# Kernel optimization log

Hardware: AMD Instinct MI355X
Metric: run time of the kernel (lower is better)

The kernel has to match this reference:

```python
import jax, jax.numpy as jnp
import numpy as np

HSS = 1024            # hidden_state_size
SEQ = 8               # mamba_seq_size (forced: HSS//SEQ*8 must equal HSS)
HID = HSS // SEQ * 8  # mamba d_model = 1024
REWARD = 2
BATCH = 256
D_INNER = 2 * HID     # mamba expand=2
HEADDIM = 64
NHEADS = D_INNER // HEADDIM
DSTATE = 128
DCONV = 4
CONV_DIM = D_INNER + 2 * DSTATE


def _mamba_layer_params(key, scale):
    k = jax.random.split(key, 5)
    d_in_proj = 2 * D_INNER + 2 * DSTATE + NHEADS
    return (
        jax.random.normal(k[0], (HID, d_in_proj)) * scale,                       # in_proj
        jax.random.normal(k[1], (CONV_DIM, DCONV)) * scale,                      # depthwise conv weight
        jnp.zeros((CONV_DIM,)),                                                  # conv bias
        jax.random.normal(k[2], (NHEADS,)) * 0.5,                                # dt_bias
        jnp.log(jax.random.uniform(k[3], (NHEADS,), minval=1.0, maxval=16.0)),   # A_log
        jnp.ones((NHEADS,)),                                                     # D skip
        jnp.ones((D_INNER,)),                                                    # gated-RMSNorm weight
        jax.random.normal(k[4], (D_INNER, HID)) * scale,                         # out_proj
    )


def setup_inputs() -> dict:
    key = jax.random.key(0)
    ks = jax.random.split(key, 8)
    s = 0.02
    inp = {"x": jax.random.normal(ks[0], (BATCH, HSS), dtype=jnp.float32)}
    inp["w_in1"] = jax.random.normal(ks[1], (HSS, HSS * SEQ)) * s
    inp["b_in1"] = jnp.zeros((HSS * SEQ,))
    inp["w_in2"] = jax.random.normal(ks[2], (HSS * SEQ, HSS * SEQ)) * s
    inp["b_in2"] = jnp.zeros((HSS * SEQ,))
    for i, k in ((1, ks[3]), (2, ks[4])):
        (inp[f"m{i}_in_proj"], inp[f"m{i}_conv_w"], inp[f"m{i}_conv_b"],
         inp[f"m{i}_dt_bias"], inp[f"m{i}_A_log"], inp[f"m{i}_D"],
         inp[f"m{i}_norm_w"], inp[f"m{i}_out_proj"]) = _mamba_layer_params(k, s)
    inp["w_out1"] = jax.random.normal(ks[5], (HID * SEQ, HID)) * s
    inp["b_out1"] = jnp.zeros((HID,))
    inp["w_out2"] = jax.random.normal(ks[6], (HID, REWARD)) * s
    inp["b_out2"] = jnp.zeros((REWARD,))
    return inp


def _mamba2(x, in_proj, conv_w, conv_b, dt_bias, A_log, Dp, norm_w, out_proj):
    # x: (B, L, HID). Mamba2 block (ngroups=1) with sequential selective scan.
    Bb, L, _ = x.shape
    zxbcdt = x @ in_proj
    z = zxbcdt[..., :D_INNER]
    xBC = zxbcdt[..., D_INNER:D_INNER + CONV_DIM]
    dt = zxbcdt[..., D_INNER + CONV_DIM:]                       # (B, L, H)
    # causal depthwise conv, kernel DCONV
    xp = jnp.pad(xBC, ((0, 0), (DCONV - 1, 0), (0, 0)))
    xBC = sum(xp[:, k:k + L, :] * conv_w[:, k] for k in range(DCONV)) + conv_b
    xBC = jax.nn.silu(xBC)
    xs = xBC[..., :D_INNER].reshape(Bb, L, NHEADS, HEADDIM)
    Bm = xBC[..., D_INNER:D_INNER + DSTATE]                     # (B, L, S)
    Cm = xBC[..., D_INNER + DSTATE:]                            # (B, L, S)
    dt = jax.nn.softplus(dt + dt_bias)
    dA = jnp.exp(dt * (-jnp.exp(A_log)))                        # (B, L, H)

    def step(h, ins):
        dA_t, dt_t, x_t, B_t, C_t = ins
        # h: (B, H, P, S)
        h = dA_t[:, :, None, None] * h + (dt_t[:, :, None] * x_t)[..., None] * B_t[:, None, None, :]
        y = jnp.einsum('bhps,bs->bhp', h, C_t)
        return h, y

    h0 = jnp.zeros((Bb, NHEADS, HEADDIM, DSTATE), x.dtype)
    ins = (dA.transpose(1, 0, 2), dt.transpose(1, 0, 2), xs.transpose(1, 0, 2, 3),
           Bm.transpose(1, 0, 2), Cm.transpose(1, 0, 2))
    _, ys = jax.lax.scan(step, h0, ins)                          # ys: (L, B, H, P)
    y = ys.transpose(1, 0, 2, 3) + xs * Dp[:, None]
    # gated RMSNorm: rmsnorm(y * silu(z)) * weight
    y = y.reshape(Bb, L, D_INNER) * jax.nn.silu(z)
    y = y * jax.lax.rsqrt(jnp.mean(y * y, axis=-1, keepdims=True) + 1e-5) * norm_w
    return y @ out_proj


def reference(x, w_in1, b_in1, w_in2, b_in2,
              m1_in_proj, m1_conv_w, m1_conv_b, m1_dt_bias, m1_A_log, m1_D, m1_norm_w, m1_out_proj,
              m2_in_proj, m2_conv_w, m2_conv_b, m2_dt_bias, m2_A_log, m2_D, m2_norm_w, m2_out_proj,
              w_out1, b_out1, w_out2, b_out2):
    b = x.shape[0]
    h = jax.nn.relu(x @ w_in1 + b_in1) @ w_in2 + b_in2          # mlp_in
    h = h.reshape(b, SEQ, HID)
    h = _mamba2(h, m1_in_proj, m1_conv_w, m1_conv_b, m1_dt_bias, m1_A_log, m1_D, m1_norm_w, m1_out_proj)
    h = _mamba2(h, m2_in_proj, m2_conv_w, m2_conv_b, m2_dt_bias, m2_A_log, m2_D, m2_norm_w, m2_out_proj)
    h = h.reshape(b, SEQ * HID)
    return jax.nn.relu(h @ w_out1 + b_out1) @ w_out2 + b_out2   # mlp_out
```

## Files before the change

kernel.cpp:

```cpp
#include <hip/hip_runtime.h>

#define BATCHN 256
#define SEQL   8
#define HIDN   1024
#define DIN    2048
#define NH     32
#define HDIM   64
#define DST    128
#define CONVD  2304
#define DPROJ  4384
#define DPROJP 4480
#define ROWS   2048

typedef float f32x4 __attribute__((ext_vector_type(4)));
typedef short bf16x8 __attribute__((ext_vector_type(8)));

__device__ __forceinline__ ushort f2bf(float f) {
    unsigned x = __float_as_uint(f);
    unsigned r = (x + 0x7fffu + ((x >> 16) & 1u)) >> 16;
    return (ushort)r;
}
__device__ __forceinline__ float bf2f(ushort u) {
    return __uint_as_float(((unsigned)u) << 16);
}

#define GL2LDS(g, l)                                                        \
    __builtin_amdgcn_global_load_lds(                                       \
        (const __attribute__((address_space(1))) void*)(g),                 \
        (__attribute__((address_space(3))) void*)(l), 16, 0, 0)

__global__ __launch_bounds__(256)
void transpose_bf16(const float* __restrict__ W, ushort* __restrict__ Wt,
                    int N, int K)
{
    __shared__ float tile[64][65];
    const int n0 = blockIdx.x * 64;
    const int k0 = blockIdx.y * 64;
    const int t  = threadIdx.x;
    const int ln = (t & 15) * 4;
    const int lk = t >> 4;
#pragma unroll
    for (int i = 0; i < 4; ++i) {
        const int k  = lk + i * 16;
        const int gn = n0 + ln;
        float4 v;
        if (gn + 3 < N) {
            v = *reinterpret_cast<const float4*>(&W[(size_t)(k0 + k) * N + gn]);
        } else {
            v.x = (gn + 0 < N) ? W[(size_t)(k0 + k) * N + gn + 0] : 0.f;
            v.y = (gn + 1 < N) ? W[(size_t)(k0 + k) * N + gn + 1] : 0.f;
            v.z = (gn + 2 < N) ? W[(size_t)(k0 + k) * N + gn + 2] : 0.f;
            v.w = (gn + 3 < N) ? W[(size_t)(k0 + k) * N + gn + 3] : 0.f;
        }
        tile[k][ln + 0] = v.x; tile[k][ln + 1] = v.y;
        tile[k][ln + 2] = v.z; tile[k][ln + 3] = v.w;
    }
    __syncthreads();
    const int wk = (t & 15) * 4;
    const int wn = t >> 4;
#pragma unroll
    for (int i = 0; i < 4; ++i) {
        const int n = wn + i * 16;
        ushort4 o;
        o.x = f2bf(tile[wk + 0][n]);
        o.y = f2bf(tile[wk + 1][n]);
        o.z = f2bf(tile[wk + 2][n]);
        o.w = f2bf(tile[wk + 3][n]);
        *reinterpret_cast<ushort4*>(&Wt[(size_t)(n0 + n) * K + k0 + wk]) = o;
    }
}

template<int OM, bool BIASF, bool RELUF>
__global__ __launch_bounds__(256)
void gemm_bf16(const ushort* __restrict__ A, int lda,
               const ushort* __restrict__ Bt, int ldb,
               const float* __restrict__ bias,
               void* __restrict__ Cv, int ldc,
               int kLen, int kchunk)
{
    __shared__ __align__(16) ushort As[128 * 32];
    __shared__ __align__(16) ushort Bs[128 * 32];
    const int t    = threadIdx.x;
    const int row0 = blockIdx.y * 128;
    const int col0 = blockIdx.x * 128;
    const int kOff = blockIdx.z * kchunk;
    const int kEnd = min(kLen, kOff + kchunk);
    const int lane = t & 63;
    const int wv   = t >> 6;
    const int wr   = wv >> 1, wc = wv & 1;
    const int frow = lane & 15;
    const int fko  = (lane >> 4) * 8;

    f32x4 acc[4][4];
#pragma unroll
    for (int m = 0; m < 4; ++m)
#pragma unroll
        for (int n = 0; n < 4; ++n) acc[m][n] = f32x4{0.f, 0.f, 0.f, 0.f};

    const int sRow = t >> 2;
    const int sCol = (t & 3) * 8;
    const ushort* aBase = A  + (size_t)(row0 + sRow) * lda + sCol;
    const ushort* bBase = Bt + (size_t)(col0 + sRow) * ldb + sCol;
    ushort* aL = As + t * 8;
    ushort* bL = Bs + t * 8;

    for (int kg = kOff; kg < kEnd; kg += 32) {
        GL2LDS(aBase + kg, aL);
        GL2LDS(aBase + (size_t)64 * lda + kg, aL + 2048);
        GL2LDS(bBase + kg, bL);
        GL2LDS(bBase + (size_t)64 * ldb + kg, bL + 2048);
        __syncthreads();
        bf16x8 af[4], bfr[4];
#pragma unroll
        for (int m = 0; m < 4; ++m)
            af[m] = *reinterpret_cast<const bf16x8*>(&As[(wr * 64 + m * 16 + frow) * 32 + fko]);
#pragma unroll
        for (int n = 0; n < 4; ++n)
            bfr[n] = *reinterpret_cast<const bf16x8*>(&Bs[(wc * 64 + n * 16 + frow) * 32 + fko]);
#pragma unroll
        for (int m = 0; m < 4; ++m)
#pragma unroll
            for (int n = 0; n < 4; ++n)
                acc[m][n] = __builtin_amdgcn_mfma_f32_16x16x32_bf16(af[m], bfr[n], acc[m][n], 0, 0, 0);
        __syncthreads();
    }

    float*  Cf = (float*)Cv;
    ushort* Cb = (ushort*)Cv;
    const int colBase = col0 + wc * 64;
    const int rowBase = row0 + wr * 64 + (lane >> 4) * 4;
#pragma unroll
    for (int n = 0; n < 4; ++n) {
        const int col = colBase + n * 16 + frow;
        const float bv = BIASF ? bias[col] : 0.f;
#pragma unroll
        for (int m = 0; m < 4; ++m) {
#pragma unroll
            for (int r = 0; r < 4; ++r) {
                const int row = rowBase + m * 16 + r;
                float v = acc[m][n][r] + bv;
                if (RELUF) v = fmaxf(v, 0.f);
                if (OM == 0)      Cf[(size_t)row * ldc + col] = v;
                else if (OM == 1) Cb[(size_t)row * ldc + col] = f2bf(v);
                else              atomicAdd(&Cf[(size_t)row * ldc + col], v);
            }
        }
    }
}

__global__ __launch_bounds__(256)
void convert_bf16(const float* __restrict__ in, ushort* __restrict__ out)
{
    int i = (blockIdx.x * 256 + threadIdx.x) * 4;
    float4 v = *reinterpret_cast<const float4*>(&in[i]);
    ushort4 o = {f2bf(v.x), f2bf(v.y), f2bf(v.z), f2bf(v.w)};
    *reinterpret_cast<ushort4*>(&out[i]) = o;
}

template<bool RELUF>
__global__ __launch_bounds__(256)
void post_bias(const float* __restrict__ acc, const float* __restrict__ bias,
               ushort* __restrict__ out, int nmask)
{
    int i = (blockIdx.x * 256 + threadIdx.x) * 4;
    float4 v = *reinterpret_cast<const float4*>(&acc[i]);
    int col = i & nmask;
    float4 b = *reinterpret_cast<const float4*>(&bias[col]);
    float r0 = v.x + b.x, r1 = v.y + b.y, r2 = v.z + b.z, r3 = v.w + b.w;
    if (RELUF) {
        r0 = fmaxf(r0, 0.f); r1 = fmaxf(r1, 0.f);
        r2 = fmaxf(r2, 0.f); r3 = fmaxf(r3, 0.f);
    }
    ushort4 o = {f2bf(r0), f2bf(r1), f2bf(r2), f2bf(r3)};
    *reinterpret_cast<ushort4*>(&out[i]) = o;
}

__global__ __launch_bounds__(256)
void conv_kernel(const float* __restrict__ zx, const float* __restrict__ cw,
                 const float* __restrict__ cb, float* __restrict__ xbc)
{
    int g = blockIdx.x * 256 + threadIdx.x;
    if (g >= BATCHN * CONVD) return;
    int c = g % CONVD;
    int b = g / CONVD;
    float x8[SEQL];
#pragma unroll
    for (int l = 0; l < SEQL; ++l)
        x8[l] = zx[(size_t)(b * SEQL + l) * DPROJP + DIN + c];
    float w0 = cw[c * 4 + 0], w1 = cw[c * 4 + 1];
    float w2 = cw[c * 4 + 2], w3 = cw[c * 4 + 3];
    float bb = cb[c];
#pragma unroll
    for (int l = 0; l < SEQL; ++l) {
        float s = bb;
        if (l >= 3) s = fmaf(w0, x8[l - 3], s);
        if (l >= 2) s = fmaf(w1, x8[l - 2], s);
        if (l >= 1) s = fmaf(w2, x8[l - 1], s);
        s = fmaf(w3, x8[l], s);
        float a = s / (1.f + __expf(-s));
        xbc[(size_t)(b * SEQL + l) * CONVD + c] = a;
    }
}

__global__ __launch_bounds__(256)
void dt_kernel(const float* __restrict__ zx, const float* __restrict__ dt_bias,
               const float* __restrict__ A_log, float* __restrict__ dtb,
               float* __restrict__ dab)
{
    int i = blockIdx.x * 256 + threadIdx.x;
    if (i >= ROWS * NH) return;
    int row = i >> 5, h = i & 31;
    float v = zx[(size_t)row * DPROJP + (DIN + CONVD) + h] + dt_bias[h];
    float dt = (v > 20.f) ? v : log1pf(__expf(v));
    float dA = __expf(-__expf(A_log[h]) * dt);
    dtb[i] = dt;
    dab[i] = dA;
}

__global__ __launch_bounds__(256)
void scan_kernel(const float* __restrict__ xbc, const float* __restrict__ dtb,
                 const float* __restrict__ dab, const float* __restrict__ Dv,
                 float* __restrict__ y)
{
    const int b  = blockIdx.x >> 5;
    const int h  = blockIdx.x & 31;
    const int t  = threadIdx.x;
    const int sc = t >> 6;
    const int p  = t & 63;
    __shared__ float BC[256];
    __shared__ float part[256];
    float st[32];
#pragma unroll
    for (int j = 0; j < 32; ++j) st[j] = 0.f;
    const float Dh = Dv[h];

    for (int l = 0; l < SEQL; ++l) {
        const int row = b * SEQL + l;
        BC[t] = xbc[(size_t)row * CONVD + DIN + t];
        __syncthreads();
        const float dA = dab[row * NH + h];
        const float dt = dtb[row * NH + h];
        const float xp = xbc[(size_t)row * CONVD + h * HDIM + p];
        const float coef = dt * xp;
        float acc = 0.f;
#pragma unroll
        for (int j = 0; j < 32; ++j) {
            const int s = sc * 32 + j;
            st[j] = fmaf(dA, st[j], coef * BC[s]);
            acc = fmaf(st[j], BC[128 + s], acc);
        }
        part[t] = acc;
        __syncthreads();
        if (sc == 0) {
            float yv = part[p] + part[64 + p] + part[128 + p] + part[192 + p];
            y[(size_t)row * DIN + h * HDIM + p] = yv + Dh * xp;
        }
    }
}

__global__ __launch_bounds__(256)
void gate_rms(const float* __restrict__ y, const float* __restrict__ zx,
              const float* __restrict__ nw, ushort* __restrict__ yb)
{
    const int row = blockIdx.x;
    const int t = threadIdx.x;
    float g[8];
    float ss = 0.f;
#pragma unroll
    for (int i = 0; i < 8; ++i) {
        int d = t + i * 256;
        float yv = y[(size_t)row * DIN + d];
        float zv = zx[(size_t)row * DPROJP + d];
        float sil = zv / (1.f + __expf(-zv));
        float gv = yv * sil;
        g[i] = gv;
        ss = fmaf(gv, gv, ss);
    }
#pragma unroll
    for (int o = 32; o >= 1; o >>= 1) ss += __shfl_xor(ss, o, 64);
    __shared__ float red[4];
    if ((t & 63) == 0) red[t >> 6] = ss;
    __syncthreads();
    float tot = red[0] + red[1] + red[2] + red[3];
    float scale = rsqrtf(tot * (1.f / DIN) + 1e-5f);
#pragma unroll
    for (int i = 0; i < 8; ++i) {
        int d = t + i * 256;
        yb[(size_t)row * DIN + d] = f2bf(g[i] * scale * nw[d]);
    }
}

__global__ __launch_bounds__(256)
void final_out(const ushort* __restrict__ f1b, const float* __restrict__ w2,
               const float* __restrict__ b2, float* __restrict__ out)
{
    int row  = blockIdx.x * 4 + (threadIdx.x >> 6);
    int lane = threadIdx.x & 63;
    float a0 = 0.f, a1 = 0.f;
#pragma unroll
    for (int i = 0; i < 16; ++i) {
        int k = lane + i * 64;
        float f = bf2f(f1b[row * 1024 + k]);
        a0 = fmaf(f, w2[k * 2 + 0], a0);
        a1 = fmaf(f, w2[k * 2 + 1], a1);
    }
#pragma unroll
    for (int o = 32; o >= 1; o >>= 1) {
        a0 += __shfl_xor(a0, o, 64);
        a1 += __shfl_xor(a1, o, 64);
    }
    if (lane == 0) {
        out[row * 2 + 0] = a0 + b2[0];
        out[row * 2 + 1] = a1 + b2[1];
    }
}

extern "C" void kernel_launch(void* const* d_in, const int* in_sizes, int n_in,
                              void* d_out, int out_size, void* d_ws, size_t ws_size,
                              hipStream_t stream)
{
    const float* x      = (const float*)d_in[0];
    const float* w_in1  = (const float*)d_in[1];
    const float* b_in1  = (const float*)d_in[2];
    const float* w_in2  = (const float*)d_in[3];
    const float* b_in2  = (const float*)d_in[4];
    const float* m_in_proj[2]  = {(const float*)d_in[5],  (const float*)d_in[13]};
    const float* m_conv_w[2]   = {(const float*)d_in[6],  (const float*)d_in[14]};
    const float* m_conv_b[2]   = {(const float*)d_in[7],  (const float*)d_in[15]};
    const float* m_dt_bias[2]  = {(const float*)d_in[8],  (const float*)d_in[16]};
    const float* m_A_log[2]    = {(const float*)d_in[9],  (const float*)d_in[17]};
    const float* m_D[2]        = {(const float*)d_in[10], (const float*)d_in[18]};
    const float* m_norm_w[2]   = {(const float*)d_in[11], (const float*)d_in[19]};
    const float* m_out_proj[2] = {(const float*)d_in[12], (const float*)d_in[20]};
    const float* w_out1 = (const float*)d_in[21];
    const float* b_out1 = (const float*)d_in[22];
    const float* w_out2 = (const float*)d_in[23];
    const float* b_out2 = (const float*)d_in[24];
    float* out = (float*)d_out;

    char* p = (char*)d_ws;
    ushort* wT   = (ushort*)p;                 p += (size_t)8192 * 2048 * 2;
    ushort* xb   = (ushort*)p;                 p += (size_t)256 * 1024 * 2;
    ushort* h1b  = (ushort*)p;                 p += (size_t)256 * 8192 * 2;
    ushort* actb = (ushort*)p;                 p += (size_t)2048 * 1024 * 2;
    float*  cacc = (float*)p;                  p += (size_t)256 * 8192 * 4;
    float*  zx   = (float*)p;                  p += (size_t)ROWS * DPROJP * 4;
    float*  xbc  = (float*)p;                  p += (size_t)ROWS * CONVD * 4;
    float*  dtb  = (float*)p;                  p += (size_t)ROWS * NH * 4;
    float*  dab  = (float*)p;                  p += (size_t)ROWS * NH * 4;
    float*  yf   = (float*)p;                  p += (size_t)ROWS * DIN * 4;
    ushort* yb   = (ushort*)p;                 p += (size_t)ROWS * DIN * 2;
    ushort* f1b  = (ushort*)p;                 p += (size_t)256 * 1024 * 2;

    convert_bf16<<<256, 256, 0, stream>>>(x, xb);

    transpose_bf16<<<dim3(8192 / 64, 1024 / 64), 256, 0, stream>>>(w_in1, wT, 8192, 1024);
    gemm_bf16<1, true, true><<<dim3(64, 2, 1), 256, 0, stream>>>(
        xb, 1024, wT, 1024, b_in1, h1b, 8192, 1024, 1024);

    hipMemsetAsync(cacc, 0, (size_t)256 * 8192 * 4, stream);
    for (int c = 0; c < 4; ++c) {
        transpose_bf16<<<dim3(8192 / 64, 2048 / 64), 256, 0, stream>>>(
            w_in2 + (size_t)c * 2048 * 8192, wT, 8192, 2048);
        gemm_bf16<2, false, false><<<dim3(64, 2, 2), 256, 0, stream>>>(
            h1b + c * 2048, 8192, wT, 2048, nullptr, cacc, 8192, 2048, 1024);
    }
    post_bias<false><<<(256 * 8192 / 4) / 256, 256, 0, stream>>>(cacc, b_in2, actb, 8191);

    for (int m = 0; m < 2; ++m) {
        transpose_bf16<<<dim3(DPROJP / 64, 1024 / 64), 256, 0, stream>>>(m_in_proj[m], wT, DPROJ, 1024);
        gemm_bf16<0, false, false><<<dim3(DPROJP / 128, 16, 1), 256, 0, stream>>>(
            actb, 1024, wT, 1024, nullptr, zx, DPROJP, 1024, 1024);

        conv_kernel<<<(BATCHN * CONVD + 255) / 256, 256, 0, stream>>>(zx, m_conv_w[m], m_conv_b[m], xbc);
        dt_kernel<<<(ROWS * NH) / 256, 256, 0, stream>>>(zx, m_dt_bias[m], m_A_log[m], dtb, dab);
        scan_kernel<<<BATCHN * NH, 256, 0, stream>>>(xbc, dtb, dab, m_D[m], yf);
        gate_rms<<<ROWS, 256, 0, stream>>>(yf, zx, m_norm_w[m], yb);

        transpose_bf16<<<dim3(1024 / 64, 2048 / 64), 256, 0, stream>>>(m_out_proj[m], wT, 1024, 2048);
        gemm_bf16<1, false, false><<<dim3(8, 16, 1), 256, 0, stream>>>(
            yb, 2048, wT, 2048, nullptr, actb, 1024, 2048, 2048);
    }

    transpose_bf16<<<dim3(1024 / 64, 8192 / 64), 256, 0, stream>>>(w_out1, wT, 1024, 8192);
    hipMemsetAsync(cacc, 0, (size_t)256 * 1024 * 4, stream);
    gemm_bf16<2, false, false><<<dim3(8, 2, 16), 256, 0, stream>>>(
        actb, 8192, wT, 8192, nullptr, cacc, 1024, 8192, 512);
    post_bias<true><<<(256 * 1024 / 4) / 256, 256, 0, stream>>>(cacc, b_out1, f1b, 1023);

    final_out<<<64, 256, 0, stream>>>(f1b, w_out2, b_out2, out);
}
```

Baseline: 1.024 ms.

## Fuse fp32 weight transpose and bf16 conversion into GEMM B-tile loading

Removes the separate transpose_bf16 pass and its workspace buffer. The GEMM now reads the fp32 row-major weights directly, converts pairs to bf16 and writes them transposed into LDS with an XOR swizzle to limit bank conflicts. This avoids writing and re-reading a bf16 weight copy in global memory and drops several launches. In exchange, the B-tile loads go through registers instead of the async global-to-LDS path, and each block reads fp32, which doubles the weight bytes loaded per tile. Split-K factors for two GEMMs are also changed.

```diff
diff --git a/kernel.cpp b/kernel.cpp
--- a/kernel.cpp
+++ b/kernel.cpp
@@ -23,60 +23,21 @@
 __device__ __forceinline__ float bf2f(ushort u) {
     return __uint_as_float(((unsigned)u) << 16);
 }
+__device__ __forceinline__ unsigned packbf(float lo, float hi) {
+    return (unsigned)f2bf(lo) | ((unsigned)f2bf(hi) << 16);
+}
 
 #define GL2LDS(g, l)                                                        \
     __builtin_amdgcn_global_load_lds(                                       \
         (const __attribute__((address_space(1))) void*)(g),                 \
         (__attribute__((address_space(3))) void*)(l), 16, 0, 0)
 
-__global__ __launch_bounds__(256)
-void transpose_bf16(const float* __restrict__ W, ushort* __restrict__ Wt,
-                    int N, int K)
-{
-    __shared__ float tile[64][65];
-    const int n0 = blockIdx.x * 64;
-    const int k0 = blockIdx.y * 64;
-    const int t  = threadIdx.x;
-    const int ln = (t & 15) * 4;
-    const int lk = t >> 4;
-#pragma unroll
-    for (int i = 0; i < 4; ++i) {
-        const int k  = lk + i * 16;
-        const int gn = n0 + ln;
-        float4 v;
-        if (gn + 3 < N) {
-            v = *reinterpret_cast<const float4*>(&W[(size_t)(k0 + k) * N + gn]);
-        } else {
-            v.x = (gn + 0 < N) ? W[(size_t)(k0 + k) * N + gn + 0] : 0.f;
-            v.y = (gn + 1 < N) ? W[(size_t)(k0 + k) * N + gn + 1] : 0.f;
-            v.z = (gn + 2 < N) ? W[(size_t)(k0 + k) * N + gn + 2] : 0.f;
-            v.w = (gn + 3 < N) ? W[(size_t)(k0 + k) * N + gn + 3] : 0.f;
-        }
-        tile[k][ln + 0] = v.x; tile[k][ln + 1] = v.y;
-        tile[k][ln + 2] = v.z; tile[k][ln + 3] = v.w;
-    }
-    __syncthreads();
-    const int wk = (t & 15) * 4;
-    const int wn = t >> 4;
-#pragma unroll
-    for (int i = 0; i < 4; ++i) {
-        const int n = wn + i * 16;
-        ushort4 o;
-        o.x = f2bf(tile[wk + 0][n]);
-        o.y = f2bf(tile[wk + 1][n]);
-        o.z = f2bf(tile[wk + 2][n]);
-        o.w = f2bf(tile[wk + 3][n]);
-        *reinterpret_cast<ushort4*>(&Wt[(size_t)(n0 + n) * K + k0 + wk]) = o;
-    }
-}
-
-template<int OM, bool BIASF, bool RELUF>
-__global__ __launch_bounds__(256)
-void gemm_bf16(const ushort* __restrict__ A, int lda,
-               const ushort* __restrict__ Bt, int ldb,
-               const float* __restrict__ bias,
-               void* __restrict__ Cv, int ldc,
-               int kLen, int kchunk)
+template<int OM, bool BIASF, bool RELUF, bool NG>
+__global__ __launch_bounds__(256)
+void gemm_fw(const ushort* __restrict__ A, int lda,
+             const float* __restrict__ W, int ldw, int Nw,
+             const float* __restrict__ bias,
+             void* __restrict__ Cv, int ldc, int kchunk)
 {
     __shared__ __align__(16) ushort As[128 * 32];
     __shared__ __align__(16) ushort Bs[128 * 32];
@@ -84,7 +45,7 @@
     const int row0 = blockIdx.y * 128;
     const int col0 = blockIdx.x * 128;
     const int kOff = blockIdx.z * kchunk;
-    const int kEnd = min(kLen, kOff + kchunk);
+    const int kEnd = kOff + kchunk;
     const int lane = t & 63;
     const int wv   = t >> 6;
     const int wr   = wv >> 1, wc = wv & 1;
@@ -99,24 +60,49 @@
 
     const int sRow = t >> 2;
     const int sCol = (t & 3) * 8;
-    const ushort* aBase = A  + (size_t)(row0 + sRow) * lda + sCol;
-    const ushort* bBase = Bt + (size_t)(col0 + sRow) * ldb + sCol;
+    const ushort* aBase = A + (size_t)(row0 + sRow) * lda + sCol;
     ushort* aL = As + t * 8;
-    ushort* bL = Bs + t * 8;
+
+    const int bn   = 4 * (t & 31);
+    const int swz  = (t & 3) << 3;
 
     for (int kg = kOff; kg < kEnd; kg += 32) {
         GL2LDS(aBase + kg, aL);
         GL2LDS(aBase + (size_t)64 * lda + kg, aL + 2048);
-        GL2LDS(bBase + kg, bL);
-        GL2LDS(bBase + (size_t)64 * ldb + kg, bL + 2048);
+#pragma unroll
+        for (int i = 0; i < 2; ++i) {
+            const int k = 2 * ((t >> 5) + i * 8);
+            const float* wp = W + (size_t)(kg + k) * ldw + col0 + bn;
+            float w0[4], w1[4];
+            if (!NG || (col0 + bn + 3 < Nw)) {
+                float4 a4 = *reinterpret_cast<const float4*>(wp);
+                float4 b4 = *reinterpret_cast<const float4*>(wp + ldw);
+                w0[0] = a4.x; w0[1] = a4.y; w0[2] = a4.z; w0[3] = a4.w;
+                w1[0] = b4.x; w1[1] = b4.y; w1[2] = b4.z; w1[3] = b4.w;
+            } else {
+#pragma unroll
+                for (int e = 0; e < 4; ++e) {
+                    const bool ok = (col0 + bn + e) < Nw;
+                    w0[e] = ok ? wp[e] : 0.f;
+                    w1[e] = ok ? wp[ldw + e] : 0.f;
+                }
+            }
+            const int kk = k ^ swz;
+#pragma unroll
+            for (int j = 0; j < 4; ++j)
+                *reinterpret_cast<unsigned*>(&Bs[(bn + j) * 32 + kk]) = packbf(w0[j], w1[j]);
+        }
         __syncthreads();
         bf16x8 af[4], bfr[4];
 #pragma unroll
         for (int m = 0; m < 4; ++m)
             af[m] = *reinterpret_cast<const bf16x8*>(&As[(wr * 64 + m * 16 + frow) * 32 + fko]);
 #pragma unroll
-        for (int n = 0; n < 4; ++n)
-            bfr[n] = *reinterpret_cast<const bf16x8*>(&Bs[(wc * 64 + n * 16 + frow) * 32 + fko]);
+        for (int n = 0; n < 4; ++n) {
+            const int row = wc * 64 + n * 16 + frow;
+            const int kkr = fko ^ (((row >> 2) & 3) << 3);
+            bfr[n] = *reinterpret_cast<const bf16x8*>(&Bs[row * 32 + kkr]);
+        }
 #pragma unroll
         for (int m = 0; m < 4; ++m)
 #pragma unroll
@@ -339,7 +325,6 @@
     float* out = (float*)d_out;
 
     char* p = (char*)d_ws;
-    ushort* wT   = (ushort*)p;                 p += (size_t)8192 * 2048 * 2;
     ushort* xb   = (ushort*)p;                 p += (size_t)256 * 1024 * 2;
     ushort* h1b  = (ushort*)p;                 p += (size_t)256 * 8192 * 2;
     ushort* actb = (ushort*)p;                 p += (size_t)2048 * 1024 * 2;
@@ -354,38 +339,30 @@
 
     convert_bf16<<<256, 256, 0, stream>>>(x, xb);
 
-    transpose_bf16<<<dim3(8192 / 64, 1024 / 64), 256, 0, stream>>>(w_in1, wT, 8192, 1024);
-    gemm_bf16<1, true, true><<<dim3(64, 2, 1), 256, 0, stream>>>(
-        xb, 1024, wT, 1024, b_in1, h1b, 8192, 1024, 1024);
+    gemm_fw<1, true, true, false><<<dim3(64, 2, 1), 256, 0, stream>>>(
+        xb, 1024, w_in1, 8192, 8192, b_in1, h1b, 8192, 1024);
 
     hipMemsetAsync(cacc, 0, (size_t)256 * 8192 * 4, stream);
-    for (int c = 0; c < 4; ++c) {
-        transpose_bf16<<<dim3(8192 / 64, 2048 / 64), 256, 0, stream>>>(
-            w_in2 + (size_t)c * 2048 * 8192, wT, 8192, 2048);
-        gemm_bf16<2, false, false><<<dim3(64, 2, 2), 256, 0, stream>>>(
-            h1b + c * 2048, 8192, wT, 2048, nullptr, cacc, 8192, 2048, 1024);
-    }
+    gemm_fw<2, false, false, false><<<dim3(64, 2, 4), 256, 0, stream>>>(
+        h1b, 8192, w_in2, 8192, 8192, nullptr, cacc, 8192, 2048);
     post_bias<false><<<(256 * 8192 / 4) / 256, 256, 0, stream>>>(cacc, b_in2, actb, 8191);
 
     for (int m = 0; m < 2; ++m) {
-        transpose_bf16<<<dim3(DPROJP / 64, 1024 / 64), 256, 0, stream>>>(m_in_proj[m], wT, DPROJ, 1024);
-        gemm_bf16<0, false, false><<<dim3(DPROJP / 128, 16, 1), 256, 0, stream>>>(
-            actb, 1024, wT, 1024, nullptr, zx, DPROJP, 1024, 1024);
+        gemm_fw<0, false, false, true><<<dim3(DPROJP / 128, 16, 1), 256, 0, stream>>>(
+            actb, 1024, m_in_proj[m], DPROJ, DPROJ, nullptr, zx, DPROJP, 1024);
 
         conv_kernel<<<(BATCHN * CONVD + 255) / 256, 256, 0, stream>>>(zx, m_conv_w[m], m_conv_b[m], xbc);
         dt_kernel<<<(ROWS * NH) / 256, 256, 0, stream>>>(zx, m_dt_bias[m], m_A_log[m], dtb, dab);
         scan_kernel<<<BATCHN * NH, 256, 0, stream>>>(xbc, dtb, dab, m_D[m], yf);
         gate_rms<<<ROWS, 256, 0, stream>>>(yf, zx, m_norm_w[m], yb);
 
-        transpose_bf16<<<dim3(1024 / 64, 2048 / 64), 256, 0, stream>>>(m_out_proj[m], wT, 1024, 2048);
-        gemm_bf16<1, false, false><<<dim3(8, 16, 1), 256, 0, stream>>>(
-            yb, 2048, wT, 2048, nullptr, actb, 1024, 2048, 2048);
-    }
-
-    transpose_bf16<<<dim3(1024 / 64, 8192 / 64), 256, 0, stream>>>(w_out1, wT, 1024, 8192);
+        gemm_fw<1, false, false, false><<<dim3(8, 16, 1), 256, 0, stream>>>(
+            yb, 2048, m_out_proj[m], 1024, 1024, nullptr, actb, 1024, 2048);
+    }
+
     hipMemsetAsync(cacc, 0, (size_t)256 * 1024 * 4, stream);
-    gemm_bf16<2, false, false><<<dim3(8, 2, 16), 256, 0, stream>>>(
-        actb, 8192, wT, 8192, nullptr, cacc, 1024, 8192, 512);
+    gemm_fw<2, false, false, false><<<dim3(8, 2, 8), 256, 0, stream>>>(
+        actb, 8192, w_out1, 1024, 1024, nullptr, cacc, 1024, 1024);
     post_bias<true><<<(256 * 1024 / 4) / 256, 256, 0, stream>>>(cacc, b_out1, f1b, 1023);
 
     final_out<<<64, 256, 0, stream>>>(f1b, w_out2, b_out2, out);
```

New measurement: 1.020 ms. About the same (-0.5%).
